# Optimization experiments

Hardware: AMD Instinct MI355X
Metric: run time of the kernel (lower is better)

The kernel has to match this reference:

```python
import jax, jax.numpy as jnp
import numpy as np

B, T, C, H = 2, 2048, 768, 12
HD = C // H  # head dim = 64


def setup_inputs() -> dict:
    key = jax.random.key(0)
    k1, k2, k3 = jax.random.split(key, 3)
    s_in = 1.0 / np.sqrt(C)
    return {
        "x": jax.random.normal(k1, (B, T, C), dtype=jnp.float32),
        "Wqkv": jax.random.normal(k2, (C, 3 * C), dtype=jnp.float32) * s_in,
        "bqkv": jnp.zeros((3 * C,), dtype=jnp.float32),
        "Wproj": jax.random.normal(k3, (C, C), dtype=jnp.float32) * s_in,
        "bproj": jnp.zeros((C,), dtype=jnp.float32),
    }


def reference(x, Wqkv, bqkv, Wproj, bproj):
    b, t, c = x.shape
    qkv = x @ Wqkv + bqkv                      # [b, t, 3c]
    q, k, v = jnp.split(qkv, 3, axis=2)
    # [b, h, t, hd]
    q = q.reshape(b, t, H, HD).transpose(0, 2, 1, 3)
    k = k.reshape(b, t, H, HD).transpose(0, 2, 1, 3)
    v = v.reshape(b, t, H, HD).transpose(0, 2, 1, 3)
    scale = 1.0 / np.sqrt(HD)
    att = jnp.einsum("bhqd,bhkd->bhqk", q, k) * scale  # [b, h, t, t]
    causal = jnp.tril(jnp.ones((t, t), dtype=bool))
    att = jnp.where(causal[None, None], att, -jnp.inf)
    att = jax.nn.softmax(att, axis=-1)
    y = jnp.einsum("bhqk,bhkd->bhqd", att, v)          # [b, h, t, hd]
    y = y.transpose(0, 2, 1, 3).reshape(b, t, c)
    return y @ Wproj + bproj
```

## Files before the change

### kernel.cpp

```cpp
#include <hip/hip_runtime.h>
#include <math.h>

#define BB 2
#define TT 2048
#define CC 768
#define HH 12
#define HD 64
#define N3 (3*CC)

typedef __attribute__((ext_vector_type(8))) short short8;
typedef __attribute__((ext_vector_type(8))) _Float16 f16x8;
typedef __attribute__((ext_vector_type(4))) float f32x4;
typedef unsigned short u16;

static __device__ __forceinline__ u16 f2h(float x) {
    union { _Float16 h; u16 u; } v; v.h = (_Float16)x; return v.u;
}

static __device__ __forceinline__ void gl16(const void* g, void* l) {
    __builtin_amdgcn_global_load_lds(
        (const __attribute__((address_space(1))) void*)g,
        (__attribute__((address_space(3))) void*)l, 16, 0, 0);
}

__global__ __launch_bounds__(256)
void conv_h(const float* __restrict__ src, u16* __restrict__ dst)
{
    const int i = blockIdx.x * 256 + threadIdx.x;
    float4 v = ((const float4*)src)[i];
    ushort4 o;
    o.x = f2h(v.x); o.y = f2h(v.y); o.z = f2h(v.z); o.w = f2h(v.w);
    ((ushort4*)dst)[i] = o;
}

__global__ __launch_bounds__(256)
void conv_th(const float* __restrict__ W, u16* __restrict__ Th, int N)
{
    __shared__ float Tt[64][65];
    const int tid = threadIdx.x;
    const int n0 = blockIdx.x * 64, k0 = blockIdx.y * 64;
    {
        const int r = tid >> 2, q = tid & 3;
        #pragma unroll
        for (int i = 0; i < 4; ++i) {
            float4 v = *(const float4*)(W + (size_t)(k0 + r) * N + n0 + q * 16 + i * 4);
            Tt[q * 16 + i * 4 + 0][r] = v.x;
            Tt[q * 16 + i * 4 + 1][r] = v.y;
            Tt[q * 16 + i * 4 + 2][r] = v.z;
            Tt[q * 16 + i * 4 + 3][r] = v.w;
        }
    }
    __syncthreads();
    {
        const int n = tid >> 2, q = tid & 3;
        u16 hh[16];
        #pragma unroll
        for (int j = 0; j < 16; ++j) hh[j] = f2h(Tt[n][q * 16 + j]);
        u16* dh = Th + (size_t)(n0 + n) * 768 + k0 + q * 16;
        *(short8*)(dh) = *(short8*)&hh[0];
        *(short8*)(dh + 8) = *(short8*)&hh[8];
    }
}

template<int NCOLS, int MODE>
__global__ __launch_bounds__(256)
void mm3(const u16* __restrict__ A_g, const u16* __restrict__ B_g,
         const float* __restrict__ bias, float* __restrict__ outF,
         u16* __restrict__ qo, u16* __restrict__ ko, u16* __restrict__ vto)
{
    __shared__ u16 gsm[16384];
    char* smb = (char*)gsm;
    const int tid = threadIdx.x, lane = tid & 63, wv = tid >> 6;
    const int wm = wv >> 1, wn = wv & 1, r16 = lane & 15, kg = lane >> 4;
    const int m0 = blockIdx.y * 128, n0 = blockIdx.x * 128;

    const u16 *pA[2], *pB[2];
    int ldsq[2];
    #pragma unroll
    for (int qq = 0; qq < 2; ++qq) {
        const int L = wv * 2048 + qq * 1024 + lane * 16;
        const int row = L >> 6, c = (L >> 4) & 3;
        const int cp = c ^ ((row >> 1) & 3);
        ldsq[qq] = wv * 2048 + qq * 1024;
        pA[qq] = A_g + (size_t)(m0 + row) * 768 + cp * 8;
        pB[qq] = B_g + (size_t)(n0 + row) * 768 + cp * 8;
    }

    int aA[4], aB[4];
    #pragma unroll
    for (int t = 0; t < 4; ++t) {
        const int rA = wm * 64 + t * 16 + r16;
        const int rB = wn * 64 + t * 16 + r16;
        aA[t] = rA * 64 + ((kg ^ ((rA >> 1) & 3)) << 4);
        aB[t] = rB * 64 + ((kg ^ ((rB >> 1) & 3)) << 4) + 8192;
    }

    f32x4 acc[4][4];
    #pragma unroll
    for (int i = 0; i < 4; ++i)
        #pragma unroll
        for (int j = 0; j < 4; ++j) acc[i][j] = (f32x4)0.f;

    #pragma unroll
    for (int qq = 0; qq < 2; ++qq) {
        gl16(pA[qq], smb + ldsq[qq]);
        gl16(pB[qq], smb + 8192 + ldsq[qq]);
        pA[qq] += 32; pB[qq] += 32;
    }
    __syncthreads();

    int cur = 0;
    for (int ks = 0; ks < 24; ++ks) {
        const int nxt = cur ^ 1;
        if (ks != 23) {
            #pragma unroll
            for (int qq = 0; qq < 2; ++qq) {
                gl16(pA[qq], smb + nxt * 16384 + ldsq[qq]);
                gl16(pB[qq], smb + nxt * 16384 + 8192 + ldsq[qq]);
                pA[qq] += 32; pB[qq] += 32;
            }
        }
        const int cb = cur * 16384;
        f16x8 a[4], b[4];
        #pragma unroll
        for (int t = 0; t < 4; ++t) {
            a[t] = *(const f16x8*)(smb + cb + aA[t]);
            b[t] = *(const f16x8*)(smb + cb + aB[t]);
        }
        #pragma unroll
        for (int mt = 0; mt < 4; ++mt)
            #pragma unroll
            for (int nt = 0; nt < 4; ++nt)
                acc[mt][nt] = __builtin_amdgcn_mfma_f32_16x16x32_f16(a[mt], b[nt], acc[mt][nt], 0, 0, 0);
        __syncthreads();
        cur = nxt;
    }

    float bi[4];
    #pragma unroll
    for (int nt = 0; nt < 4; ++nt) bi[nt] = bias[n0 + wn * 64 + nt * 16 + r16];

    if (MODE == 1) {
        #pragma unroll
        for (int mt = 0; mt < 4; ++mt)
            #pragma unroll
            for (int nt = 0; nt < 4; ++nt)
                #pragma unroll
                for (int r = 0; r < 4; ++r) {
                    const int grow = m0 + wm * 64 + mt * 16 + kg * 4 + r;
                    const int gcol = n0 + wn * 64 + nt * 16 + r16;
                    outF[(size_t)grow * CC + gcol] = acc[mt][nt][r] + bi[nt];
                }
    } else {
        const int which = n0 / CC;
        const int b_ = m0 >> 11;
        #pragma unroll
        for (int mt = 0; mt < 4; ++mt) {
            const int tb = ((m0 & 2047) + wm * 64 + mt * 16 + kg * 4);
            #pragma unroll
            for (int nt = 0; nt < 4; ++nt) {
                const int gcol = n0 + wn * 64 + nt * 16 + r16;
                const int cc = gcol - which * CC;
                const int h = cc >> 6, d = cc & 63;
                const int bh_ = b_ * HH + h;
                if (which == 2) {
                    ushort4 hv;
                    #pragma unroll
                    for (int r = 0; r < 4; ++r)
                        ((u16*)&hv)[r] = f2h(acc[mt][nt][r] + bi[nt]);
                    *(ushort4*)(vto + ((size_t)bh_ * 64 + d) * 2048 + tb) = hv;
                } else {
                    u16* dst = (which == 0) ? qo : ko;
                    #pragma unroll
                    for (int r = 0; r < 4; ++r)
                        dst[(((size_t)bh_ * 2048 + tb + r) << 6) + d] =
                            f2h(acc[mt][nt][r] + bi[nt]);
                }
            }
        }
    }
}

__global__ __launch_bounds__(256)
void attn3(const u16* __restrict__ qp, const u16* __restrict__ kp,
           const u16* __restrict__ vtp, u16* __restrict__ attp)
{
    __shared__ u16 smem[20480];
    char* smb = (char*)smem;

    const int tid = threadIdx.x, bid = blockIdx.x;
    const int qt = 31 - (bid / 24);
    const int bh = bid % 24;
    const int lane = tid & 63, wv = tid >> 6;
    const int r16 = lane & 15, kg = lane >> 4;

    const size_t qro = ((size_t)bh * TT + qt * 64 + wv * 16 + r16) * 64;
    f16x8 qf[2];
    #pragma unroll
    for (int ks = 0; ks < 2; ++ks)
        qf[ks] = *(const f16x8*)(qp + qro + ks * 32 + kg * 8);

    const u16 *pk[2], *pv[2];
    int ldsq[2];
    #pragma unroll
    for (int qq = 0; qq < 2; ++qq) {
        const int L = wv * 2048 + qq * 1024 + lane * 16;
        const int row = L >> 7, c = (L >> 4) & 7;
        const int cp = c ^ (row & 7);
        ldsq[qq] = wv * 2048 + qq * 1024;
        pk[qq] = kp + ((size_t)bh * TT + row) * 64 + cp * 8;
        pv[qq] = vtp + ((size_t)bh * 64 + row) * TT + cp * 8;
    }

    int aK[2][4], aP[2];
    #pragma unroll
    for (int ks = 0; ks < 2; ++ks) {
        #pragma unroll
        for (int nt = 0; nt < 4; ++nt) {
            const int row = nt * 16 + r16;
            aK[ks][nt] = row * 128 + (((ks * 4 + kg) ^ (row & 7)) << 4);
        }
        aP[ks] = 32768 + wv * 2048 + r16 * 128 + (((ks * 4 + kg) ^ (r16 & 7)) << 4);
    }
    int pwb[4], pwx[4];
    #pragma unroll
    for (int r = 0; r < 4; ++r) {
        const int prow = kg * 4 + r;
        pwb[r] = 32768 + wv * 2048 + prow * 128;
        pwx[r] = (prow & 7) << 3;
    }

    f32x4 o_acc[4];
    #pragma unroll
    for (int i = 0; i < 4; ++i) o_acc[i] = (f32x4)0.f;
    float m_s[4] = {-1e30f, -1e30f, -1e30f, -1e30f};
    float l_s[4] = {0.f, 0.f, 0.f, 0.f};

    #pragma unroll
    for (int qq = 0; qq < 2; ++qq) {
        gl16(pk[qq], smb + ldsq[qq]);
        gl16(pv[qq], smb + 8192 + ldsq[qq]);
        pk[qq] += 4096; pv[qq] += 64;
    }
    __syncthreads();

    int cur = 0;
    for (int j = 0; j <= qt; ++j) {
        const int nxt = cur ^ 1;
        if (j != qt) {
            #pragma unroll
            for (int qq = 0; qq < 2; ++qq) {
                gl16(pk[qq], smb + nxt * 16384 + ldsq[qq]);
                gl16(pv[qq], smb + nxt * 16384 + 8192 + ldsq[qq]);
                pk[qq] += 4096; pv[qq] += 64;
            }
        }
        const int cb = cur * 16384;

        f32x4 s[4];
        #pragma unroll
        for (int nt = 0; nt < 4; ++nt) s[nt] = (f32x4)0.f;
        #pragma unroll
        for (int ks = 0; ks < 2; ++ks)
            #pragma unroll
            for (int nt = 0; nt < 4; ++nt) {
                f16x8 kf = *(const f16x8*)(smb + cb + aK[ks][nt]);
                s[nt] = __builtin_amdgcn_mfma_f32_16x16x32_f16(qf[ks], kf, s[nt], 0, 0, 0);
            }
        #pragma unroll
        for (int nt = 0; nt < 4; ++nt) s[nt] *= 0.125f;

        if (j == qt) {
            #pragma unroll
            for (int nt = 0; nt < 4; ++nt)
                #pragma unroll
                for (int r = 0; r < 4; ++r)
                    if (nt * 16 + r16 > wv * 16 + kg * 4 + r) s[nt][r] = -1e30f;
        }

        #pragma unroll
        for (int r = 0; r < 4; ++r) {
            float mx = fmaxf(fmaxf(s[0][r], s[1][r]), fmaxf(s[2][r], s[3][r]));
            mx = fmaxf(mx, __shfl_xor(mx, 1));
            mx = fmaxf(mx, __shfl_xor(mx, 2));
            mx = fmaxf(mx, __shfl_xor(mx, 4));
            mx = fmaxf(mx, __shfl_xor(mx, 8));
            const float mn = fmaxf(m_s[r], mx);
            const float corr = __expf(m_s[r] - mn);
            float ps = 0.f;
            #pragma unroll
            for (int nt = 0; nt < 4; ++nt) {
                const float p = __expf(s[nt][r] - mn);
                s[nt][r] = p;
                ps += p;
            }
            ps += __shfl_xor(ps, 1);
            ps += __shfl_xor(ps, 2);
            ps += __shfl_xor(ps, 4);
            ps += __shfl_xor(ps, 8);
            l_s[r] = l_s[r] * corr + ps;
            m_s[r] = mn;
            #pragma unroll
            for (int nt = 0; nt < 4; ++nt) o_acc[nt][r] *= corr;
        }

        #pragma unroll
        for (int nt = 0; nt < 4; ++nt)
            #pragma unroll
            for (int r = 0; r < 4; ++r)
                *(u16*)(smb + pwb[r] + (((nt * 16 + r16) ^ pwx[r]) << 1)) = f2h(s[nt][r]);

        #pragma unroll
        for (int ks = 0; ks < 2; ++ks) {
            f16x8 pa = *(const f16x8*)(smb + aP[ks]);
            #pragma unroll
            for (int nt = 0; nt < 4; ++nt) {
                f16x8 vf = *(const f16x8*)(smb + cb + 8192 + aK[ks][nt]);
                o_acc[nt] = __builtin_amdgcn_mfma_f32_16x16x32_f16(pa, vf, o_acc[nt], 0, 0, 0);
            }
        }

        __syncthreads();
        cur = nxt;
    }

    const int b_ = bh / HH, h = bh % HH;
    #pragma unroll
    for (int r = 0; r < 4; ++r) {
        const float inv = 1.f / l_s[r];
        const int t = qt * 64 + wv * 16 + kg * 4 + r;
        const size_t base = ((size_t)b_ * TT + t) * CC + h * 64;
        #pragma unroll
        for (int nt = 0; nt < 4; ++nt)
            attp[base + nt * 16 + r16] = f2h(o_acc[nt][r] * inv);
    }
}

extern "C" void kernel_launch(void* const* d_in, const int* in_sizes, int n_in,
                              void* d_out, int out_size, void* d_ws, size_t ws_size,
                              hipStream_t stream)
{
    const float* x     = (const float*)d_in[0];
    const float* Wqkv  = (const float*)d_in[1];
    const float* bqkv  = (const float*)d_in[2];
    const float* Wproj = (const float*)d_in[3];
    const float* bproj = (const float*)d_in[4];
    float* out = (float*)d_out;

    const size_t E  = (size_t)4096 * 768;
    const size_t WQ = (size_t)2304 * 768;
    const size_t WP = (size_t)768 * 768;

    u16* ws   = (u16*)d_ws;
    u16* xh   = ws;
    u16* atth = ws;
    u16* wqh  = ws + E;
    u16* wph  = wqh + WQ;
    u16* qh   = wph + WP;
    u16* kh   = qh + E;
    u16* vth  = kh + E;

    conv_h<<<dim3((int)(E / 4 / 256)), 256, 0, stream>>>(x, xh);
    conv_th<<<dim3(N3 / 64, CC / 64), 256, 0, stream>>>(Wqkv, wqh, N3);
    conv_th<<<dim3(CC / 64, CC / 64), 256, 0, stream>>>(Wproj, wph, CC);

    mm3<N3, 0><<<dim3(N3 / 128, 32), 256, 0, stream>>>(
        xh, wqh, bqkv, nullptr, qh, kh, vth);
    attn3<<<dim3(768), 256, 0, stream>>>(qh, kh, vth, atth);
    mm3<CC, 1><<<dim3(CC / 128, 32), 256, 0, stream>>>(
        atth, wph, bproj, out, nullptr, nullptr, nullptr);
}
```

Before: 181.0 us.

## Restructure attention softmax with transposed scores, exp2, lazy rescaling, MFMA row sums

The softmax scale and log2(e) factor are folded into Q during the QKV GEMM epilogue, so the attention kernel can use exp2 directly. The QK^T MFMA operands are swapped so each lane holds one query row's scores, which reduces the row max to two cross-lane shuffles. Accumulator rescaling is skipped unless some lane's max grows by more than 8 (in log2 units), and the row sum l is computed by an extra MFMA against a ones vector instead of shuffle reductions. P is written to shared memory as packed half pairs, and s_setprio hints are placed around the MFMA blocks. Together these aim to cut VALU, shuffle and LDS-store overhead, at the cost of an extra MFMA per k-step and looser numerical headroom from the lazy max.

```diff
diff --git a/kernel.cpp b/kernel.cpp
--- a/kernel.cpp
+++ b/kernel.cpp
@@ -13,8 +13,21 @@
 typedef __attribute__((ext_vector_type(4))) float f32x4;
 typedef unsigned short u16;
 
+#define QSCALE 0.1803368809f
+
 static __device__ __forceinline__ u16 f2h(float x) {
     union { _Float16 h; u16 u; } v; v.h = (_Float16)x; return v.u;
+}
+static __device__ __forceinline__ float ex2(float x) {
+#if __has_builtin(__builtin_amdgcn_exp2f)
+    return __builtin_amdgcn_exp2f(x);
+#else
+    return exp2f(x);
+#endif
+}
+static __device__ __forceinline__ unsigned pk2h(float a, float b) {
+    auto p = __builtin_amdgcn_cvt_pkrtz(a, b);
+    return __builtin_bit_cast(unsigned, p);
 }
 
 static __device__ __forceinline__ void gl16(const void* g, void* l) {
@@ -153,6 +166,7 @@
                 }
     } else {
         const int which = n0 / CC;
+        const float qsc = (which == 0) ? QSCALE : 1.0f;
         const int b_ = m0 >> 11;
         #pragma unroll
         for (int mt = 0; mt < 4; ++mt) {
@@ -174,7 +188,7 @@
                     #pragma unroll
                     for (int r = 0; r < 4; ++r)
                         dst[(((size_t)bh_ * 2048 + tb + r) << 6) + d] =
-                            f2h(acc[mt][nt][r] + bi[nt]);
+                            f2h((acc[mt][nt][r] + bi[nt]) * qsc);
                 }
             }
         }
@@ -193,6 +207,7 @@
     const int bh = bid % 24;
     const int lane = tid & 63, wv = tid >> 6;
     const int r16 = lane & 15, kg = lane >> 4;
+    const int r7 = r16 & 7;
 
     const size_t qro = ((size_t)bh * TT + qt * 64 + wv * 16 + r16) * 64;
     f16x8 qf[2];
@@ -220,21 +235,20 @@
             const int row = nt * 16 + r16;
             aK[ks][nt] = row * 128 + (((ks * 4 + kg) ^ (row & 7)) << 4);
         }
-        aP[ks] = 32768 + wv * 2048 + r16 * 128 + (((ks * 4 + kg) ^ (r16 & 7)) << 4);
-    }
-    int pwb[4], pwx[4];
-    #pragma unroll
-    for (int r = 0; r < 4; ++r) {
-        const int prow = kg * 4 + r;
-        pwb[r] = 32768 + wv * 2048 + prow * 128;
-        pwx[r] = (prow & 7) << 3;
-    }
+        aP[ks] = 32768 + wv * 2048 + r16 * 128 + (((ks * 4 + kg) ^ r7) << 4);
+    }
+    const int pwbase = 32768 + wv * 2048 + r16 * 128;
+    const int kg8 = kg * 8, kg4 = kg * 4;
 
     f32x4 o_acc[4];
     #pragma unroll
     for (int i = 0; i < 4; ++i) o_acc[i] = (f32x4)0.f;
-    float m_s[4] = {-1e30f, -1e30f, -1e30f, -1e30f};
-    float l_s[4] = {0.f, 0.f, 0.f, 0.f};
+    f32x4 o_l = (f32x4)0.f;
+    float m = -1e30f;
+
+    f16x8 ones;
+    #pragma unroll
+    for (int i = 0; i < 8; ++i) ones[i] = (_Float16)1.0f;
 
     #pragma unroll
     for (int qq = 0; qq < 2; ++qq) {
@@ -260,65 +274,71 @@
         f32x4 s[4];
         #pragma unroll
         for (int nt = 0; nt < 4; ++nt) s[nt] = (f32x4)0.f;
+        __builtin_amdgcn_s_setprio(1);
         #pragma unroll
         for (int ks = 0; ks < 2; ++ks)
             #pragma unroll
             for (int nt = 0; nt < 4; ++nt) {
                 f16x8 kf = *(const f16x8*)(smb + cb + aK[ks][nt]);
-                s[nt] = __builtin_amdgcn_mfma_f32_16x16x32_f16(qf[ks], kf, s[nt], 0, 0, 0);
-            }
-        #pragma unroll
-        for (int nt = 0; nt < 4; ++nt) s[nt] *= 0.125f;
+                s[nt] = __builtin_amdgcn_mfma_f32_16x16x32_f16(kf, qf[ks], s[nt], 0, 0, 0);
+            }
+        __builtin_amdgcn_s_setprio(0);
 
         if (j == qt) {
             #pragma unroll
             for (int nt = 0; nt < 4; ++nt)
                 #pragma unroll
                 for (int r = 0; r < 4; ++r)
-                    if (nt * 16 + r16 > wv * 16 + kg * 4 + r) s[nt][r] = -1e30f;
-        }
-
-        #pragma unroll
-        for (int r = 0; r < 4; ++r) {
-            float mx = fmaxf(fmaxf(s[0][r], s[1][r]), fmaxf(s[2][r], s[3][r]));
-            mx = fmaxf(mx, __shfl_xor(mx, 1));
-            mx = fmaxf(mx, __shfl_xor(mx, 2));
-            mx = fmaxf(mx, __shfl_xor(mx, 4));
-            mx = fmaxf(mx, __shfl_xor(mx, 8));
-            const float mn = fmaxf(m_s[r], mx);
-            const float corr = __expf(m_s[r] - mn);
-            float ps = 0.f;
+                    if (nt * 16 + kg4 + r > wv * 16 + r16) s[nt][r] = -1e30f;
+        }
+
+        float pm = s[0][0];
+        #pragma unroll
+        for (int nt = 0; nt < 4; ++nt)
+            #pragma unroll
+            for (int r = 0; r < 4; ++r)
+                if (nt | r) pm = fmaxf(pm, s[nt][r]);
+        pm = fmaxf(pm, __shfl_xor(pm, 16));
+        pm = fmaxf(pm, __shfl_xor(pm, 32));
+
+        if (__any(pm > m + 8.0f)) {
+            const float mn = fmaxf(m, pm);
+            const float corr = ex2(m - mn);
+            m = mn;
+            const float c0 = __shfl(corr, kg4 + 0);
+            const float c1 = __shfl(corr, kg4 + 1);
+            const float c2 = __shfl(corr, kg4 + 2);
+            const float c3 = __shfl(corr, kg4 + 3);
             #pragma unroll
             for (int nt = 0; nt < 4; ++nt) {
-                const float p = __expf(s[nt][r] - mn);
-                s[nt][r] = p;
-                ps += p;
-            }
-            ps += __shfl_xor(ps, 1);
-            ps += __shfl_xor(ps, 2);
-            ps += __shfl_xor(ps, 4);
-            ps += __shfl_xor(ps, 8);
-            l_s[r] = l_s[r] * corr + ps;
-            m_s[r] = mn;
-            #pragma unroll
-            for (int nt = 0; nt < 4; ++nt) o_acc[nt][r] *= corr;
-        }
-
-        #pragma unroll
-        for (int nt = 0; nt < 4; ++nt)
-            #pragma unroll
-            for (int r = 0; r < 4; ++r)
-                *(u16*)(smb + pwb[r] + (((nt * 16 + r16) ^ pwx[r]) << 1)) = f2h(s[nt][r]);
-
+                o_acc[nt][0] *= c0; o_acc[nt][1] *= c1;
+                o_acc[nt][2] *= c2; o_acc[nt][3] *= c3;
+            }
+            o_l[0] *= c0; o_l[1] *= c1; o_l[2] *= c2; o_l[3] *= c3;
+        }
+
+        #pragma unroll
+        for (int nt = 0; nt < 4; ++nt) {
+            const float p0 = ex2(s[nt][0] - m), p1 = ex2(s[nt][1] - m);
+            const float p2 = ex2(s[nt][2] - m), p3 = ex2(s[nt][3] - m);
+            uint2 w;
+            w.x = pk2h(p0, p1);
+            w.y = pk2h(p2, p3);
+            *(uint2*)(smb + pwbase + ((nt * 32 + kg8) ^ (r7 << 4))) = w;
+        }
+
+        __builtin_amdgcn_s_setprio(1);
         #pragma unroll
         for (int ks = 0; ks < 2; ++ks) {
             f16x8 pa = *(const f16x8*)(smb + aP[ks]);
+            o_l = __builtin_amdgcn_mfma_f32_16x16x32_f16(pa, ones, o_l, 0, 0, 0);
             #pragma unroll
             for (int nt = 0; nt < 4; ++nt) {
                 f16x8 vf = *(const f16x8*)(smb + cb + 8192 + aK[ks][nt]);
                 o_acc[nt] = __builtin_amdgcn_mfma_f32_16x16x32_f16(pa, vf, o_acc[nt], 0, 0, 0);
             }
         }
+        __builtin_amdgcn_s_setprio(0);
 
         __syncthreads();
         cur = nxt;
@@ -327,8 +347,8 @@
     const int b_ = bh / HH, h = bh % HH;
     #pragma unroll
     for (int r = 0; r < 4; ++r) {
-        const float inv = 1.f / l_s[r];
-        const int t = qt * 64 + wv * 16 + kg * 4 + r;
+        const float inv = 1.f / o_l[r];
+        const int t = qt * 64 + wv * 16 + kg4 + r;
         const size_t base = ((size_t)b_ * TT + t) * CC + h * 64;
         #pragma unroll
         for (int nt = 0; nt < 4; ++nt)
```

Result: faster. 156.2 us (-13.7%).
